# Kernel optimization log

Hardware: AMD Instinct MI355X
Metric: run time of the kernel (lower is better)

Reference implementation:

```python
import jax, jax.numpy as jnp
import numpy as np

HIDDEN = 246


def _gcn_conv(x, W, b, src, dst, norm, n_nodes):
    # PyG GCNConv: linear (no bias) -> normalized neighbor aggregation -> + bias
    h = x @ W                                   # [N, C_out]
    msg = h[src] * norm[:, None]                # [E', C_out]
    agg = jax.ops.segment_sum(msg, dst, num_segments=n_nodes)
    return agg + b


def setup_inputs() -> dict:
    key = jax.random.key(0)
    ks = jax.random.split(key, 10)
    N, F_IN, E = 50000, 256, 320000
    x = jax.random.normal(ks[0], (N, F_IN), dtype=jnp.float32)
    edge_index = jax.random.randint(ks[1], (2, E), 0, N, dtype=jnp.int64)
    def glorot(k, fan_in, fan_out):
        s = jnp.sqrt(2.0 / (fan_in + fan_out)).astype(jnp.float32)
        return jax.random.normal(k, (fan_in, fan_out), dtype=jnp.float32) * s
    return {
        "x": x,
        "edge_index": edge_index,
        "W1": glorot(ks[2], F_IN, HIDDEN), "b1": jnp.zeros((HIDDEN,), jnp.float32),
        "W2": glorot(ks[3], HIDDEN, HIDDEN), "b2": jnp.zeros((HIDDEN,), jnp.float32),
        "W3": glorot(ks[4], HIDDEN, HIDDEN), "b3": jnp.zeros((HIDDEN,), jnp.float32),
        "W4": glorot(ks[5], HIDDEN, HIDDEN), "b4": jnp.zeros((HIDDEN,), jnp.float32),
    }


def reference(x, edge_index, W1, b1, W2, b2, W3, b3, W4, b4):
    N = x.shape[0]
    src, dst = edge_index[0], edge_index[1]
    # add self-loops (edge_weight=None -> all-ones weights)
    loops = jnp.arange(N, dtype=edge_index.dtype)
    src_f = jnp.concatenate([src, loops])
    dst_f = jnp.concatenate([dst, loops])
    # symmetric GCN normalization: D^{-1/2} (A+I) D^{-1/2}
    deg = jax.ops.segment_sum(jnp.ones_like(src_f, dtype=x.dtype), dst_f, num_segments=N)
    dinv = jnp.where(deg > 0, jax.lax.rsqrt(jnp.maximum(deg, 1.0)), 0.0)
    norm = dinv[src_f] * dinv[dst_f]            # [E+N]

    h = jax.nn.relu(_gcn_conv(x, W1, b1, src_f, dst_f, norm, N))
    h = jax.nn.relu(_gcn_conv(h, W2, b2, src_f, dst_f, norm, N))
    h = jax.nn.relu(_gcn_conv(h, W3, b3, src_f, dst_f, norm, N))
    h = _gcn_conv(h, W4, b4, src_f, dst_f, norm, N)
    # NOTE: original forward never calls conv5; log_softmax over hidden dim,
    # faithfully reproduced. Dropout is identity in eval mode.
    return jax.nn.log_softmax(h, axis=1)
```

## Files before the change

### kernel.cpp

```cpp
#include <hip/hip_runtime.h>
#include <cstdint>
#include <cstddef>


typedef __bf16 bf16x8 __attribute__((ext_vector_type(8)));
typedef float f32x4 __attribute__((ext_vector_type(4)));

__device__ __forceinline__ unsigned short f2bf(float v) {
    union { float f; unsigned u; } x; x.f = v;
    unsigned r = x.u + 0x7fff + ((x.u >> 16) & 1);
    return (unsigned short)(r >> 16);
}
__device__ __forceinline__ float bf2f(unsigned short h) {
    union { unsigned u; float f; } x; x.u = (unsigned)h << 16; return x.f;
}

__device__ __forceinline__ void gl2lds16(const void* g, void* l) {
    __builtin_amdgcn_global_load_lds(
        (const __attribute__((address_space(1))) unsigned int*)g,
        (__attribute__((address_space(3))) unsigned int*)l, 16, 0, 0);
}

__device__ __forceinline__ void fma4(const uint2 v, float n, float* acc) {
    acc[0] += bf2f((unsigned short)(v.x & 0xffff)) * n;
    acc[1] += bf2f((unsigned short)(v.x >> 16)) * n;
    acc[2] += bf2f((unsigned short)(v.y & 0xffff)) * n;
    acc[3] += bf2f((unsigned short)(v.y >> 16)) * n;
}

__global__ void k_flag_init(int* flag) {
    if (blockIdx.x == 0 && threadIdx.x == 0) *flag = 1;
}

__global__ void k_flag_check(const long long* __restrict__ p, int E, long long N,
                             int* flag) {
    long long i = (long long)blockIdx.x * blockDim.x + threadIdx.x;
    long long stride = (long long)gridDim.x * blockDim.x;
    for (; i < E; i += stride) {
        long long v = p[i];
        if (v < 0 || v >= N) *flag = 0;
    }
}

__device__ __forceinline__ void load_edge(const void* eidx, int fl, int E, int i,
                                          int& s, int& d) {
    if (fl) {
        s = (int)((const long long*)eidx)[i];
        d = (int)((const long long*)eidx)[E + i];
    } else {
        s = ((const int*)eidx)[i];
        d = ((const int*)eidx)[E + i];
    }
}

__global__ void k_zero_i32(int* __restrict__ p, int n) {
    int i = blockIdx.x * blockDim.x + threadIdx.x;
    if (i < n) p[i] = 0;
}

__global__ void k_count(const void* __restrict__ eidx, const int* __restrict__ flag,
                        int* __restrict__ counts, int E) {
    int i = blockIdx.x * blockDim.x + threadIdx.x;
    if (i >= E) return;
    int s, d;
    load_edge(eidx, *flag, E, i, s, d);
    atomicAdd(&counts[d], 1);
}

__global__ void k_dinv(const int* __restrict__ counts, float* __restrict__ dinv,
                       int N) {
    int i = blockIdx.x * blockDim.x + threadIdx.x;
    if (i < N) dinv[i] = rsqrtf((float)counts[i] + 1.0f);
}

__global__ __launch_bounds__(1024) void k_scan(const int* __restrict__ counts,
                                               int* __restrict__ starts, int N) {
    __shared__ int wsum[16];
    __shared__ int wscan[16];
    __shared__ int s_carry;
    int tid = threadIdx.x;
    int lane = tid & 63, wid = tid >> 6;
    if (tid == 0) s_carry = 0;
    __syncthreads();
    for (int base = 0; base < N; base += 1024) {
        int i = base + tid;
        int v = (i < N) ? counts[i] : 0;
        int incl = v;
#pragma unroll
        for (int off = 1; off < 64; off <<= 1) {
            int t = __shfl_up(incl, off);
            if (lane >= off) incl += t;
        }
        if (lane == 63) wsum[wid] = incl;
        __syncthreads();
        if (wid == 0 && lane < 16) {
            int w = wsum[lane];
#pragma unroll
            for (int off = 1; off < 16; off <<= 1) {
                int t = __shfl_up(w, off);
                if (lane >= off) w += t;
            }
            wscan[lane] = w;
        }
        __syncthreads();
        int woff = (wid > 0) ? wscan[wid - 1] : 0;
        int excl = s_carry + woff + incl - v;
        if (i < N) starts[i] = excl;
        int total = wscan[15];
        __syncthreads();
        if (tid == 0) s_carry += total;
        __syncthreads();
    }
    if (tid == 0) starts[N] = s_carry;
}

__global__ void k_copy_i32(const int* __restrict__ a, int* __restrict__ b, int n) {
    int i = blockIdx.x * blockDim.x + threadIdx.x;
    if (i < n) b[i] = a[i];
}

__global__ void k_fill(const void* __restrict__ eidx, const int* __restrict__ flag,
                       int* __restrict__ cursor, int* __restrict__ srcs, int E) {
    int i = blockIdx.x * blockDim.x + threadIdx.x;
    if (i >= E) return;
    int s, d;
    load_edge(eidx, *flag, E, i, s, d);
    int pos = atomicAdd(&cursor[d], 1);
    srcs[pos] = s;
}

__global__ void k_cvt_x(const float* __restrict__ x, unsigned short* __restrict__ o,
                        long long n4) {
    long long i = (long long)blockIdx.x * blockDim.x + threadIdx.x;
    long long stride = (long long)gridDim.x * blockDim.x;
    for (; i < n4; i += stride) {
        float4 v = ((const float4*)x)[i];
        unsigned a = (unsigned)f2bf(v.x) | ((unsigned)f2bf(v.y) << 16);
        unsigned b = (unsigned)f2bf(v.z) | ((unsigned)f2bf(v.w) << 16);
        ((uint2*)o)[i] = make_uint2(a, b);
    }
}

__global__ void k_cvt_w(const float* __restrict__ W, unsigned short* __restrict__ T,
                        int K, int H) {
    int idx = blockIdx.x * blockDim.x + threadIdx.x;
    if (idx >= 256 * 256) return;
    int k = idx & 255, n = idx >> 8;
    float v = (k < K && n < H) ? W[k * H + n] : 0.0f;
    T[n * 256 + k] = f2bf(v);
}

__global__ __launch_bounds__(256) void k_gemm_mfma(
        const unsigned short* __restrict__ A,
        const unsigned short* __restrict__ BT,
        unsigned short* __restrict__ C, int M) {
    __shared__ unsigned short ldsA[4 * 128 * 8];
    __shared__ unsigned short ldsB[4 * 128 * 8];

    int tid = threadIdx.x;
    int lane = tid & 63;
    int w = tid >> 6;
    int wm = (w & 1) * 64, wn = (w >> 1) * 64;
    int kq = lane >> 4, lr = lane & 15;
    int row0 = blockIdx.y * 128, col0 = blockIdx.x * 128;

    f32x4 acc[4][4] = {};

    for (int k0 = 0; k0 < 256; k0 += 32) {
        __syncthreads();
#pragma unroll
        for (int i = 0; i < 2; i++) {
            int c = (i * 4 + w) * 64 + lane;
            int m = c & 127, kqq = c >> 7;
            int row = row0 + m; if (row >= M) row = M - 1;
            gl2lds16(&A[(long long)row * 256 + k0 + kqq * 8],
                     &ldsA[(i * 4 + w) * 512]);
        }
#pragma unroll
        for (int i = 0; i < 2; i++) {
            int c = (i * 4 + w) * 64 + lane;
            int n = c & 127, kqq = c >> 7;
            gl2lds16(&BT[(long long)(col0 + n) * 256 + k0 + kqq * 8],
                     &ldsB[(i * 4 + w) * 512]);
        }
        __syncthreads();

        bf16x8 a[4], b[4];
#pragma unroll
        for (int t = 0; t < 4; t++) {
            int m = wm + t * 16 + lr;
            a[t] = *(const bf16x8*)&ldsA[(kq * 128 + m) * 8];
            int n = wn + t * 16 + lr;
            b[t] = *(const bf16x8*)&ldsB[(kq * 128 + n) * 8];
        }
#pragma unroll
        for (int mt = 0; mt < 4; mt++)
#pragma unroll
            for (int nt = 0; nt < 4; nt++)
                acc[mt][nt] = __builtin_amdgcn_mfma_f32_16x16x32_bf16(
                    a[mt], b[nt], acc[mt][nt], 0, 0, 0);
    }

#pragma unroll
    for (int mt = 0; mt < 4; mt++) {
#pragma unroll
        for (int nt = 0; nt < 4; nt++) {
            int col = col0 + wn + nt * 16 + lr;
            int rowb = row0 + wm + mt * 16 + kq * 4;
#pragma unroll
            for (int r = 0; r < 4; r++) {
                int row = rowb + r;
                if (row < M) C[(long long)row * 256 + col] = f2bf(acc[mt][nt][r]);
            }
        }
    }
}

__device__ __forceinline__ void agg_rows(
        const unsigned short* __restrict__ h,
        const int* __restrict__ srcs, const int* __restrict__ starts,
        const float* __restrict__ dinv, int d, int f0, float dd, float* acc) {
    int lane = threadIdx.x & 63;
    int e0 = starts[d], e1 = starts[d + 1];
    int cnt = e1 - e0;
    int cpre = cnt < 64 ? cnt : 64;

    acc[0] = acc[1] = acc[2] = acc[3] = 0.0f;
    {
        uint2 v = *(const uint2*)&h[((long long)d << 8) + f0];
        fma4(v, dd, acc);
    }
    int sv = 0; float nv = 0.0f;
    if (lane < cpre) { sv = srcs[e0 + lane]; nv = dinv[sv]; }

    for (int base = 0; base < cpre; base += 8) {
        uint2 vv[8]; float nn[8];
#pragma unroll
        for (int t = 0; t < 8; t++) {
            int j = base + t;
            int s = __shfl(sv, j);
            float n = __shfl(nv, j);
            if (j >= cpre) { s = d; n = 0.0f; }
            nn[t] = n;
            vv[t] = *(const uint2*)&h[((long long)s << 8) + f0];
        }
#pragma unroll
        for (int t = 0; t < 8; t++) fma4(vv[t], nn[t], acc);
    }
    for (int e = e0 + 64; e < e1; e++) {
        int s0 = srcs[e];
        float n0 = dinv[s0];
        uint2 v0 = *(const uint2*)&h[((long long)s0 << 8) + f0];
        fma4(v0, n0, acc);
    }
}

__global__ __launch_bounds__(256) void k_gather_bf16(
        const unsigned short* __restrict__ h,
        const int* __restrict__ srcs, const int* __restrict__ starts,
        const float* __restrict__ dinv, const float* __restrict__ bias,
        unsigned short* __restrict__ out, int N, int H) {
    int d = blockIdx.x * 4 + (threadIdx.x >> 6);
    if (d >= N) return;
    int lane = threadIdx.x & 63;
    int f0 = lane * 4;
    float dd = dinv[d];

    float acc[4];
    agg_rows(h, srcs, starts, dinv, d, f0, dd, acc);

    unsigned short o[4];
#pragma unroll
    for (int t = 0; t < 4; t++) {
        int f = f0 + t;
        float bb = (f < H) ? bias[f] : 0.0f;
        float v = fmaxf(acc[t] * dd + bb, 0.0f);
        o[t] = f2bf(v);
    }
    unsigned o01 = (unsigned)o[0] | ((unsigned)o[1] << 16);
    unsigned o23 = (unsigned)o[2] | ((unsigned)o[3] << 16);
    *(uint2*)&out[((long long)d << 8) + f0] = make_uint2(o01, o23);
}

__global__ __launch_bounds__(256) void k_gather_lsm(
        const unsigned short* __restrict__ h,
        const int* __restrict__ srcs, const int* __restrict__ starts,
        const float* __restrict__ dinv, const float* __restrict__ bias,
        float* __restrict__ out, int N, int H) {
    int d = blockIdx.x * 4 + (threadIdx.x >> 6);
    if (d >= N) return;
    int lane = threadIdx.x & 63;
    int f0 = lane * 4;
    float dd = dinv[d];

    float acc[4];
    agg_rows(h, srcs, starts, dinv, d, f0, dd, acc);

    float v[4];
    float m = -INFINITY;
#pragma unroll
    for (int t = 0; t < 4; t++) {
        int f = f0 + t;
        float bb = (f < H) ? bias[f] : 0.0f;
        v[t] = acc[t] * dd + bb;
        if (f < H) m = fmaxf(m, v[t]);
    }
#pragma unroll
    for (int off = 32; off > 0; off >>= 1) m = fmaxf(m, __shfl_xor(m, off));
    float s = 0.0f;
#pragma unroll
    for (int t = 0; t < 4; t++) {
        int f = f0 + t;
        if (f < H) s += __expf(v[t] - m);
    }
#pragma unroll
    for (int off = 32; off > 0; off >>= 1) s += __shfl_xor(s, off);
    float lse = m + logf(s);
#pragma unroll
    for (int t = 0; t < 4; t++) {
        int f = f0 + t;
        if (f < H) out[(long long)d * H + f] = v[t] - lse;
    }
}

extern "C" void kernel_launch(void* const* d_in, const int* in_sizes, int n_in,
                              void* d_out, int out_size, void* d_ws, size_t ws_size,
                              hipStream_t stream) {
    const float* x    = (const float*)d_in[0];
    const void*  eidx = d_in[1];
    const float* W[4] = {(const float*)d_in[2], (const float*)d_in[4],
                         (const float*)d_in[6], (const float*)d_in[8]};
    const float* b[4] = {(const float*)d_in[3], (const float*)d_in[5],
                         (const float*)d_in[7], (const float*)d_in[9]};

    const int H   = in_sizes[3];
    const int E   = in_sizes[1] / 2;
    const int FIN = in_sizes[2] / H;
    const int N   = in_sizes[0] / FIN;

    auto align = [](size_t v) { return (v + 255) / 256 * 256; };
    char* ws = (char*)d_ws;
    size_t off = 0;
    int* flag = (int*)(ws + off);             off += 256;
    float* dinv = (float*)(ws + off);         off += align((size_t)N * 4);
    int* counts = (int*)(ws + off);           off += align((size_t)N * 4);
    int* starts = (int*)(ws + off);           off += align((size_t)(N + 1) * 4);
    int* srcs = (int*)(ws + off);             off += align((size_t)E * 4);
    unsigned short* Wt[4];
    for (int l = 0; l < 4; l++) {
        Wt[l] = (unsigned short*)(ws + off);  off += 256 * 256 * 2;
    }
    size_t actB = align((size_t)N * 256 * 2);
    unsigned short* A0 = (unsigned short*)(ws + off);  off += actB;
    unsigned short* A1 = (unsigned short*)(ws + off);  off += actB;
    unsigned short* Cb = (unsigned short*)(ws + off);  off += actB;

    int nb = (N + 255) / 256, eb = (E + 255) / 256;

    k_flag_init<<<1, 64, 0, stream>>>(flag);
    k_flag_check<<<512, 256, 0, stream>>>((const long long*)eidx, E, (long long)N, flag);

    k_zero_i32<<<nb, 256, 0, stream>>>(counts, N);
    k_count<<<eb, 256, 0, stream>>>(eidx, flag, counts, E);
    k_dinv<<<nb, 256, 0, stream>>>(counts, dinv, N);
    k_scan<<<1, 1024, 0, stream>>>(counts, starts, N);
    k_copy_i32<<<nb, 256, 0, stream>>>(starts, counts, N);
    k_fill<<<eb, 256, 0, stream>>>(eidx, flag, counts, srcs, E);

    k_cvt_w<<<256, 256, 0, stream>>>(W[0], Wt[0], FIN, H);
    for (int l = 1; l < 4; l++)
        k_cvt_w<<<256, 256, 0, stream>>>(W[l], Wt[l], H, H);
    k_cvt_x<<<1024, 256, 0, stream>>>(x, A0, (long long)N * FIN / 4);

    dim3 ggrid(2, (N + 127) / 128);
    int gb = (N + 3) / 4;

    k_gemm_mfma<<<ggrid, 256, 0, stream>>>(A0, Wt[0], Cb, N);
    k_gather_bf16<<<gb, 256, 0, stream>>>(Cb, srcs, starts, dinv, b[0], A1, N, H);
    k_gemm_mfma<<<ggrid, 256, 0, stream>>>(A1, Wt[1], Cb, N);
    k_gather_bf16<<<gb, 256, 0, stream>>>(Cb, srcs, starts, dinv, b[1], A0, N, H);
    k_gemm_mfma<<<ggrid, 256, 0, stream>>>(A0, Wt[2], Cb, N);
    k_gather_bf16<<<gb, 256, 0, stream>>>(Cb, srcs, starts, dinv, b[2], A1, N, H);
    k_gemm_mfma<<<ggrid, 256, 0, stream>>>(A1, Wt[3], Cb, N);
    k_gather_lsm<<<gb, 256, 0, stream>>>(Cb, srcs, starts, dinv, b[3],
                                         (float*)d_out, N, H);
}
```

Baseline: 469.5 us.

## Parallelize prefix scan, precompute per-edge norms, remap GEMM tiles per XCD

Replaces the single-block serial scan over node counts with a three-stage scan: per-block sums, a scan over those sums, then a final per-block scan. The fill kernel now stores dinv[src] per CSR edge so the gather kernels read norms contiguously instead of doing a dependent random load. The GEMM now uses a 1D grid whose block IDs are remapped so consecutive tiles land on the same XCD, aiming for better L2 reuse. Adds an E-sized workspace array and two extra small launches.

```diff
diff --git a/kernel.cpp b/kernel.cpp
--- a/kernel.cpp
+++ b/kernel.cpp
@@ -71,6 +71,29 @@
                        int N) {
     int i = blockIdx.x * blockDim.x + threadIdx.x;
     if (i < N) dinv[i] = rsqrtf((float)counts[i] + 1.0f);
+}
+
+__global__ __launch_bounds__(256) void k_bsum(const int* __restrict__ counts,
+                                              int* __restrict__ bsum, int N) {
+    __shared__ int ws[4];
+    int tid = threadIdx.x, lane = tid & 63, wid = tid >> 6;
+    int base = blockIdx.x * 1024 + tid * 4;
+    int s = 0;
+    if (base + 3 < N) {
+        int4 v = *(const int4*)&counts[base];
+        s = v.x + v.y + v.z + v.w;
+    } else {
+#pragma unroll
+        for (int t = 0; t < 4; t++) {
+            int i = base + t;
+            if (i < N) s += counts[i];
+        }
+    }
+#pragma unroll
+    for (int off = 32; off > 0; off >>= 1) s += __shfl_xor(s, off);
+    if (lane == 0) ws[wid] = s;
+    __syncthreads();
+    if (tid == 0) bsum[blockIdx.x] = ws[0] + ws[1] + ws[2] + ws[3];
 }
 
 __global__ __launch_bounds__(1024) void k_scan(const int* __restrict__ counts,
@@ -114,19 +137,57 @@
     if (tid == 0) starts[N] = s_carry;
 }
 
+__global__ __launch_bounds__(256) void k_scan_final(
+        const int* __restrict__ counts, const int* __restrict__ boffs,
+        int* __restrict__ starts, int N) {
+    __shared__ int ws[4];
+    int tid = threadIdx.x, lane = tid & 63, wid = tid >> 6;
+    int base = blockIdx.x * 1024 + tid * 4;
+    int v[4];
+#pragma unroll
+    for (int t = 0; t < 4; t++) {
+        int i = base + t;
+        v[t] = (i < N) ? counts[i] : 0;
+    }
+    int tsum = v[0] + v[1] + v[2] + v[3];
+    int incl = tsum;
+#pragma unroll
+    for (int off = 1; off < 64; off <<= 1) {
+        int t = __shfl_up(incl, off);
+        if (lane >= off) incl += t;
+    }
+    if (lane == 63) ws[wid] = incl;
+    __syncthreads();
+    int woff = 0;
+#pragma unroll
+    for (int w = 0; w < 4; w++)
+        if (w < wid) woff += ws[w];
+    int run = boffs[blockIdx.x] + woff + incl - tsum;
+#pragma unroll
+    for (int t = 0; t < 4; t++) {
+        int i = base + t;
+        if (i < N) starts[i] = run;
+        run += v[t];
+    }
+    if (blockIdx.x == 0 && tid == 0) starts[N] = boffs[gridDim.x];
+}
+
 __global__ void k_copy_i32(const int* __restrict__ a, int* __restrict__ b, int n) {
     int i = blockIdx.x * blockDim.x + threadIdx.x;
     if (i < n) b[i] = a[i];
 }
 
 __global__ void k_fill(const void* __restrict__ eidx, const int* __restrict__ flag,
-                       int* __restrict__ cursor, int* __restrict__ srcs, int E) {
+                       int* __restrict__ cursor, int* __restrict__ srcs,
+                       float* __restrict__ nrm, const float* __restrict__ dinv,
+                       int E) {
     int i = blockIdx.x * blockDim.x + threadIdx.x;
     if (i >= E) return;
     int s, d;
     load_edge(eidx, *flag, E, i, s, d);
     int pos = atomicAdd(&cursor[d], 1);
     srcs[pos] = s;
+    nrm[pos] = dinv[s];
 }
 
 __global__ void k_cvt_x(const float* __restrict__ x, unsigned short* __restrict__ o,
@@ -157,12 +218,19 @@
     __shared__ unsigned short ldsA[4 * 128 * 8];
     __shared__ unsigned short ldsB[4 * 128 * 8];
 
+    int g = blockIdx.x, nwg = gridDim.x;
+    int q = nwg >> 3, r = nwg & 7;
+    int xcd = g & 7, slot = g >> 3;
+    int work = (xcd < r) ? xcd * (q + 1) + slot
+                         : r * (q + 1) + (xcd - r) * q + slot;
+    int col0 = (work & 1) * 128;
+    int row0 = (work >> 1) * 128;
+
     int tid = threadIdx.x;
     int lane = tid & 63;
     int w = tid >> 6;
     int wm = (w & 1) * 64, wn = (w >> 1) * 64;
     int kq = lane >> 4, lr = lane & 15;
-    int row0 = blockIdx.y * 128, col0 = blockIdx.x * 128;
 
     f32x4 acc[4][4] = {};
 
@@ -208,9 +276,9 @@
             int col = col0 + wn + nt * 16 + lr;
             int rowb = row0 + wm + mt * 16 + kq * 4;
 #pragma unroll
-            for (int r = 0; r < 4; r++) {
-                int row = rowb + r;
-                if (row < M) C[(long long)row * 256 + col] = f2bf(acc[mt][nt][r]);
+            for (int r2 = 0; r2 < 4; r2++) {
+                int row = rowb + r2;
+                if (row < M) C[(long long)row * 256 + col] = f2bf(acc[mt][nt][r2]);
             }
         }
     }
@@ -218,8 +286,8 @@
 
 __device__ __forceinline__ void agg_rows(
         const unsigned short* __restrict__ h,
-        const int* __restrict__ srcs, const int* __restrict__ starts,
-        const float* __restrict__ dinv, int d, int f0, float dd, float* acc) {
+        const int* __restrict__ srcs, const float* __restrict__ nrm,
+        const int* __restrict__ starts, int d, int f0, float dd, float* acc) {
     int lane = threadIdx.x & 63;
     int e0 = starts[d], e1 = starts[d + 1];
     int cnt = e1 - e0;
@@ -231,7 +299,7 @@
         fma4(v, dd, acc);
     }
     int sv = 0; float nv = 0.0f;
-    if (lane < cpre) { sv = srcs[e0 + lane]; nv = dinv[sv]; }
+    if (lane < cpre) { sv = srcs[e0 + lane]; nv = nrm[e0 + lane]; }
 
     for (int base = 0; base < cpre; base += 8) {
         uint2 vv[8]; float nn[8];
@@ -249,7 +317,7 @@
     }
     for (int e = e0 + 64; e < e1; e++) {
         int s0 = srcs[e];
-        float n0 = dinv[s0];
+        float n0 = nrm[e];
         uint2 v0 = *(const uint2*)&h[((long long)s0 << 8) + f0];
         fma4(v0, n0, acc);
     }
@@ -257,7 +325,8 @@
 
 __global__ __launch_bounds__(256) void k_gather_bf16(
         const unsigned short* __restrict__ h,
-        const int* __restrict__ srcs, const int* __restrict__ starts,
+        const int* __restrict__ srcs, const float* __restrict__ nrm,
+        const int* __restrict__ starts,
         const float* __restrict__ dinv, const float* __restrict__ bias,
         unsigned short* __restrict__ out, int N, int H) {
     int d = blockIdx.x * 4 + (threadIdx.x >> 6);
@@ -267,7 +336,7 @@
     float dd = dinv[d];
 
     float acc[4];
-    agg_rows(h, srcs, starts, dinv, d, f0, dd, acc);
+    agg_rows(h, srcs, nrm, starts, d, f0, dd, acc);
 
     unsigned short o[4];
 #pragma unroll
@@ -284,7 +353,8 @@
 
 __global__ __launch_bounds__(256) void k_gather_lsm(
         const unsigned short* __restrict__ h,
-        const int* __restrict__ srcs, const int* __restrict__ starts,
+        const int* __restrict__ srcs, const float* __restrict__ nrm,
+        const int* __restrict__ starts,
         const float* __restrict__ dinv, const float* __restrict__ bias,
         float* __restrict__ out, int N, int H) {
     int d = blockIdx.x * 4 + (threadIdx.x >> 6);
@@ -294,7 +364,7 @@
     float dd = dinv[d];
 
     float acc[4];
-    agg_rows(h, srcs, starts, dinv, d, f0, dd, acc);
+    agg_rows(h, srcs, nrm, starts, d, f0, dd, acc);
 
     float v[4];
     float m = -INFINITY;
@@ -346,6 +416,10 @@
     int* counts = (int*)(ws + off);           off += align((size_t)N * 4);
     int* starts = (int*)(ws + off);           off += align((size_t)(N + 1) * 4);
     int* srcs = (int*)(ws + off);             off += align((size_t)E * 4);
+    float* nrm = (float*)(ws + off);          off += align((size_t)E * 4);
+    int nb2 = (N + 1023) / 1024;
+    int* bsum = (int*)(ws + off);             off += align((size_t)(nb2 + 1) * 4);
+    int* boffs = (int*)(ws + off);            off += align((size_t)(nb2 + 1) * 4);
     unsigned short* Wt[4];
     for (int l = 0; l < 4; l++) {
         Wt[l] = (unsigned short*)(ws + off);  off += 256 * 256 * 2;
@@ -363,25 +437,27 @@
     k_zero_i32<<<nb, 256, 0, stream>>>(counts, N);
     k_count<<<eb, 256, 0, stream>>>(eidx, flag, counts, E);
     k_dinv<<<nb, 256, 0, stream>>>(counts, dinv, N);
-    k_scan<<<1, 1024, 0, stream>>>(counts, starts, N);
+    k_bsum<<<nb2, 256, 0, stream>>>(counts, bsum, N);
+    k_scan<<<1, 1024, 0, stream>>>(bsum, boffs, nb2);
+    k_scan_final<<<nb2, 256, 0, stream>>>(counts, boffs, starts, N);
     k_copy_i32<<<nb, 256, 0, stream>>>(starts, counts, N);
-    k_fill<<<eb, 256, 0, stream>>>(eidx, flag, counts, srcs, E);
+    k_fill<<<eb, 256, 0, stream>>>(eidx, flag, counts, srcs, nrm, dinv, E);
 
     k_cvt_w<<<256, 256, 0, stream>>>(W[0], Wt[0], FIN, H);
     for (int l = 1; l < 4; l++)
         k_cvt_w<<<256, 256, 0, stream>>>(W[l], Wt[l], H, H);
     k_cvt_x<<<1024, 256, 0, stream>>>(x, A0, (long long)N * FIN / 4);
 
-    dim3 ggrid(2, (N + 127) / 128);
+    int ggrid = 2 * ((N + 127) / 128);
     int gb = (N + 3) / 4;
 
     k_gemm_mfma<<<ggrid, 256, 0, stream>>>(A0, Wt[0], Cb, N);
-    k_gather_bf16<<<gb, 256, 0, stream>>>(Cb, srcs, starts, dinv, b[0], A1, N, H);
+    k_gather_bf16<<<gb, 256, 0, stream>>>(Cb, srcs, nrm, starts, dinv, b[0], A1, N, H);
     k_gemm_mfma<<<ggrid, 256, 0, stream>>>(A1, Wt[1], Cb, N);
-    k_gather_bf16<<<gb, 256, 0, stream>>>(Cb, srcs, starts, dinv, b[1], A0, N, H);
+    k_gather_bf16<<<gb, 256, 0, stream>>>(Cb, srcs, nrm, starts, dinv, b[1], A0, N, H);
     k_gemm_mfma<<<ggrid, 256, 0, stream>>>(A0, Wt[2], Cb, N);
-    k_gather_bf16<<<gb, 256, 0, stream>>>(Cb, srcs, starts, dinv, b[2], A1, N, H);
+    k_gather_bf16<<<gb, 256, 0, stream>>>(Cb, srcs, nrm, starts, dinv, b[2], A1, N, H);
     k_gemm_mfma<<<ggrid, 256, 0, stream>>>(A1, Wt[3], Cb, N);
-    k_gather_lsm<<<gb, 256, 0, stream>>>(Cb, srcs, starts, dinv, b[3],
+    k_gather_lsm<<<gb, 256, 0, stream>>>(Cb, srcs, nrm, starts, dinv, b[3],
                                          (float*)d_out, N, H);
 }
```

After: 421.6 us. 10.2% less time.
